# Kernel optimization log

Hardware: AMD Instinct MI355X
Metric: run time of the kernel (lower is better)

Reference implementation:

```python
import jax, jax.numpy as jnp
import numpy as np

N = 8192        # nodes
IN_F = 256      # in_features
OUT_F = 64      # out_features per head
HEADS = 4
ALPHA = 0.2     # leaky relu slope
NEG_INF = -9e15


def setup_inputs() -> dict:
    key = jax.random.key(0)
    ks = jax.random.split(key, 8)
    h = jax.random.normal(ks[0], (N, IN_F), dtype=jnp.float32)
    adj = jax.random.randint(ks[1], (N, N), 0, 2, dtype=jnp.int32)
    # per-head GAT params, stacked over heads
    W = jax.random.normal(ks[2], (HEADS, IN_F, OUT_F), dtype=jnp.float32) * (1.0 / np.sqrt(IN_F))
    a1 = jax.random.normal(ks[3], (HEADS, OUT_F), dtype=jnp.float32) * (1.0 / np.sqrt(OUT_F))
    a2 = jax.random.normal(ks[4], (HEADS, OUT_F), dtype=jnp.float32) * (1.0 / np.sqrt(OUT_F))
    # fusing linear: Linear(out*heads, out)
    fc_w = jax.random.normal(ks[5], (OUT_F, HEADS * OUT_F), dtype=jnp.float32) * (1.0 / np.sqrt(HEADS * OUT_F))
    fc_b = jax.random.normal(ks[6], (OUT_F,), dtype=jnp.float32) * 0.01
    return {"h": h, "adj": adj, "W": W, "a1": a1, "a2": a2, "fc_w": fc_w, "fc_b": fc_b}


def reference(h, adj, W, a1, a2, fc_w, fc_b):
    # all heads batched: Wh [H, N, F]
    Wh = jnp.einsum('ni,hio->hno', h, W)
    # attention logits e_ij = leakyrelu(a1.Wh_i + a2.Wh_j), shape [H, N, N]
    e_src = jnp.einsum('hno,ho->hn', Wh, a1)   # [H, N]
    e_dst = jnp.einsum('hno,ho->hn', Wh, a2)   # [H, N]
    e = jax.nn.leaky_relu(e_src[:, :, None] + e_dst[:, None, :], ALPHA)
    e = jnp.where(adj[None] > 0, e, NEG_INF)
    attn = jax.nn.softmax(e, axis=-1)          # masked softmax over neighbors
    out = jnp.einsum('hnm,hmo->hno', attn, Wh)  # [H, N, F]
    out = jax.nn.elu(out)
    # concat heads along feature dim -> [N, H*F], then fuse linear
    h_concat = jnp.transpose(out, (1, 0, 2)).reshape(N, HEADS * OUT_F)
    return h_concat @ fc_w.T + fc_b
```

## Files before the change

### kernel.cpp

```cpp
#include <hip/hip_runtime.h>
#include <hip/hip_bf16.h>

#define NN 8192
#define NHEADS 4
#define OUTF 64
#define NCHUNK 2
#define CHUNK 4096
#define ROWS 32
#define LOG2E 1.4426950408889634f

typedef __bf16 bf16x8 __attribute__((ext_vector_type(8)));
typedef float fx4 __attribute__((ext_vector_type(4)));
typedef unsigned short ushort8 __attribute__((ext_vector_type(8)));

__global__ __launch_bounds__(256) void k_bits(
    const int* __restrict__ adj, unsigned* __restrict__ bm)
{
  const int lane = threadIdx.x & 63;
  const int row = blockIdx.x * 4 + (threadIdx.x >> 6);
  const int* ap = adj + (size_t)row * NN;
  unsigned* bp = bm + (size_t)row * (NN / 32);

  for (int it8 = 0; it8 < 16; ++it8) {
    int v[8];
#pragma unroll
    for (int u = 0; u < 8; ++u)
      v[u] = ap[(it8 * 8 + u) * 64 + lane];
#pragma unroll
    for (int u = 0; u < 8; ++u) {
      unsigned long long m = __ballot(v[u] != 0);
      unsigned word = (lane == 1) ? (unsigned)(m >> 32) : (unsigned)m;
      if (lane < 2) bp[(it8 * 8 + u) * 2 + lane] = word;
    }
  }
}

__global__ __launch_bounds__(256) void k_wh(
    const float* __restrict__ h, const float* __restrict__ W,
    const float* __restrict__ a1, const float* __restrict__ a2,
    unsigned short* __restrict__ whsw, float* __restrict__ R,
    float* __restrict__ F1, float* __restrict__ F2)
{
  __shared__ float ws[64 * 260];
  const int tid = threadIdx.x;
  const int hd = blockIdx.x >> 7;
  const int i0 = (blockIdx.x & 127) << 6;

  const float* Wp = W + hd * (256 * 64);
  for (int idx = tid; idx < 256 * 64; idx += 256) {
    int k = idx >> 6, o = idx & 63;
    ws[o * 260 + k] = Wp[idx];
  }
  __syncthreads();

  const int w = tid >> 6, o = tid & 63;
  const int ibase = i0 + w * 16;
  float acc[16];
#pragma unroll
  for (int m = 0; m < 16; ++m) acc[m] = 0.f;

  const float* hp = h + (size_t)ibase * 256;
  for (int k4 = 0; k4 < 64; ++k4) {
    fx4 wv = *(const fx4*)(&ws[o * 260 + k4 * 4]);
#pragma unroll
    for (int m = 0; m < 16; ++m) {
      fx4 hv = *(const fx4*)(hp + m * 256 + k4 * 4);
      acc[m] += hv[0] * wv[0] + hv[1] * wv[1] + hv[2] * wv[2] + hv[3] * wv[3];
    }
  }

  const float a1v = a1[hd * 64 + o], a2v = a2[hd * 64 + o];
#pragma unroll
  for (int m = 0; m < 16; ++m) {
    float s1 = acc[m] * a1v, s2 = acc[m] * a2v;
#pragma unroll
    for (int d = 1; d < 64; d <<= 1) {
      s1 += __shfl_xor(s1, d);
      s2 += __shfl_xor(s2, d);
    }
    if (o == 0) {
      int ix = hd * NN + ibase + m;
      R[ix]  = __builtin_amdgcn_exp2f(-0.8f * s1 * LOG2E);
      F1[ix] = __builtin_amdgcn_exp2f(s2 * LOG2E);
      F2[ix] = __builtin_amdgcn_exp2f(0.2f * s2 * LOG2E);
    }
  }

  size_t base = (size_t)hd * 524288 + (size_t)((i0 >> 5) + (w >> 1)) * 2048 +
                (size_t)(o >> 4) * 512;
  int ln0 = (o & 15) + 16 * ((w & 1) * 2);
  ushort8 pk0, pk1;
#pragma unroll
  for (int m = 0; m < 8; ++m) {
    pk0[m] = __builtin_bit_cast(unsigned short, (__bf16)acc[m]);
    pk1[m] = __builtin_bit_cast(unsigned short, (__bf16)acc[m + 8]);
  }
  *(ushort8*)(whsw + base + (size_t)ln0 * 8) = pk0;
  *(ushort8*)(whsw + base + (size_t)(ln0 + 16) * 8) = pk1;
}

struct Tile {
  fx4 f1a, f1b, f2a, f2b;
  bf16x8 b0, b1, b2, b3;
  unsigned m[2];
};

__device__ __forceinline__ void load_tile(Tile& t, const float* F1p,
                                          const float* F2p,
                                          const unsigned short* wp,
                                          const unsigned* bml, int il, int jb)
{
  t.f1a = *(const fx4*)(F1p + jb);
  t.f1b = *(const fx4*)(F1p + jb + 4);
  t.f2a = *(const fx4*)(F2p + jb);
  t.f2b = *(const fx4*)(F2p + jb + 4);
  const unsigned short* wq = wp + (size_t)(jb >> 5) * 2048;
  t.b0 = *(const bf16x8*)(wq);
  t.b1 = *(const bf16x8*)(wq + 512);
  t.b2 = *(const bf16x8*)(wq + 1024);
  t.b3 = *(const bf16x8*)(wq + 1536);
  const int jw = jb >> 5;
  t.m[0] = bml[jw * 32 + (il ^ (jw & 31))];
  t.m[1] = bml[jw * 32 + ((16 + il) ^ (jw & 31))];
}

__device__ __forceinline__ void compute_tile(const Tile& t, const float* Rr,
                                             int g, const bf16x8& ones,
                                             fx4 acc[2][4], fx4* accS)
{
#pragma unroll
  for (int rs = 0; rs < 2; ++rs) {
    unsigned sm = t.m[rs] >> (g * 8);
    float p[8];
#pragma unroll
    for (int e = 0; e < 8; ++e) {
      float f1 = (e < 4) ? t.f1a[e] : t.f1b[e - 4];
      float f2 = (e < 4) ? t.f2a[e] : t.f2b[e - 4];
      float pm = fmaxf(f1, Rr[rs] * f2);
      unsigned keep = (unsigned)(((int)(sm << (31 - e))) >> 31);
      p[e] = __builtin_bit_cast(float,
                 __builtin_bit_cast(unsigned, pm) & keep);
    }
    bf16x8 af;
#pragma unroll
    for (int e = 0; e < 8; ++e) af[e] = (__bf16)p[e];
    acc[rs][0] = __builtin_amdgcn_mfma_f32_16x16x32_bf16(af, t.b0, acc[rs][0], 0, 0, 0);
    acc[rs][1] = __builtin_amdgcn_mfma_f32_16x16x32_bf16(af, t.b1, acc[rs][1], 0, 0, 0);
    acc[rs][2] = __builtin_amdgcn_mfma_f32_16x16x32_bf16(af, t.b2, acc[rs][2], 0, 0, 0);
    acc[rs][3] = __builtin_amdgcn_mfma_f32_16x16x32_bf16(af, t.b3, acc[rs][3], 0, 0, 0);
    accS[rs] = __builtin_amdgcn_mfma_f32_16x16x32_bf16(af, ones, accS[rs], 0, 0, 0);
  }
}

__global__ __launch_bounds__(256) void k_attn(
    const unsigned* __restrict__ bm, const unsigned short* __restrict__ whsw,
    const float* __restrict__ Rg, const float* __restrict__ F1g,
    const float* __restrict__ F2g, float* __restrict__ pacc,
    float* __restrict__ psum)
{
  __shared__ unsigned bml[(CHUNK / 32) * ROWS];
  const int tid = threadIdx.x;
  const int lane = tid & 63;
  const int hd = tid >> 6;
  const int bx = blockIdx.x;
  const int ci = bx & 1;
  const int i0 = (bx >> 1) << 5;
  const int j0 = ci * CHUNK;
  const int il = lane & 15;
  const int g = lane >> 4;

  for (int it = 0; it < 16; ++it) {
    int idx = it * 256 + tid;
    int r = idx >> 7, w = idx & 127;
    unsigned v = bm[(size_t)(i0 + r) * (NN / 32) + (j0 >> 5) + w];
    bml[w * 32 + (r ^ (w & 31))] = v;
  }
  __syncthreads();

  float Rr[2];
#pragma unroll
  for (int rs = 0; rs < 2; ++rs)
    Rr[rs] = Rg[hd * NN + i0 + rs * 16 + il];
  const float* F1p = F1g + hd * NN + j0 + g * 8;
  const float* F2p = F2g + hd * NN + j0 + g * 8;
  const unsigned short* wp = whsw + (size_t)hd * 524288 +
                             (size_t)(j0 >> 5) * 2048 + (size_t)lane * 8;
  bf16x8 ones;
#pragma unroll
  for (int e = 0; e < 8; ++e) ones[e] = (__bf16)1.0f;

  fx4 acc[2][4] = {};
  fx4 accS[2] = {};

  Tile t0, t1;
  load_tile(t0, F1p, F2p, wp, bml, il, 0);
  for (int jb = 0; jb < CHUNK; jb += 64) {
    load_tile(t1, F1p, F2p, wp, bml, il, jb + 32);
    compute_tile(t0, Rr, g, ones, acc, accS);
    if (jb + 64 < CHUNK) load_tile(t0, F1p, F2p, wp, bml, il, jb + 64);
    compute_tile(t1, Rr, g, ones, acc, accS);
  }

#pragma unroll
  for (int rs = 0; rs < 2; ++rs) {
    if (il == 0) {
#pragma unroll
      for (int r = 0; r < 4; ++r)
        psum[(size_t)(ci * NHEADS + hd) * NN + i0 + rs * 16 + g * 4 + r] =
            accS[rs][r];
    }
  }

  float* pc = pacc + (size_t)ci * NN * 256;
#pragma unroll
  for (int rs = 0; rs < 2; ++rs)
#pragma unroll
    for (int r = 0; r < 4; ++r)
#pragma unroll
      for (int ft = 0; ft < 4; ++ft)
        pc[(size_t)(i0 + rs * 16 + g * 4 + r) * 256 + hd * 64 + ft * 16 + il] =
            acc[rs][ft][r];
}

__global__ __launch_bounds__(256) void k_fc(
    const float* __restrict__ pacc, const float* __restrict__ psum,
    const float* __restrict__ fcw, const float* __restrict__ fcb,
    float* __restrict__ out)
{
  __shared__ float ws[256 * 65];
  __shared__ float ash[32 * 260];
  __shared__ float inv[32 * 4];
  const int tid = threadIdx.x;
  const int i0 = blockIdx.x * 32;

  for (int idx = tid; idx < 64 * 256; idx += 256) {
    int o = idx >> 8, c = idx & 255;
    ws[c * 65 + o] = fcw[idx];
  }
  if (tid < 128) {
    int m = tid >> 2, hh = tid & 3;
    float s = 0.f;
#pragma unroll
    for (int ci = 0; ci < NCHUNK; ++ci)
      s += psum[(size_t)(ci * NHEADS + hh) * NN + i0 + m];
    inv[m * 4 + hh] = 1.0f / s;
  }
  __syncthreads();

  for (int idx = tid; idx < 32 * 64; idx += 256) {
    int m = idx >> 6, q = idx & 63;
    int hh = q >> 4;
    size_t off = (size_t)(i0 + m) * 256 + q * 4;
    fx4 v = {};
#pragma unroll
    for (int ci = 0; ci < NCHUNK; ++ci) {
      fx4 a = *(const fx4*)(pacc + (size_t)ci * NN * 256 + off);
      v[0] += a[0]; v[1] += a[1]; v[2] += a[2]; v[3] += a[3];
    }
    float iv = inv[m * 4 + hh];
#pragma unroll
    for (int j = 0; j < 4; ++j) {
      float x = v[j] * iv;
      x = (x > 0.f) ? x : (__builtin_amdgcn_exp2f(x * LOG2E) - 1.0f);
      ash[m * 260 + q * 4 + j] = x;
    }
  }
  __syncthreads();

  const int w = tid >> 6, o = tid & 63;
  float acc[8];
#pragma unroll
  for (int m = 0; m < 8; ++m) acc[m] = 0.f;

  for (int c4 = 0; c4 < 64; ++c4) {
    float w0 = ws[(c4 * 4 + 0) * 65 + o];
    float w1 = ws[(c4 * 4 + 1) * 65 + o];
    float w2 = ws[(c4 * 4 + 2) * 65 + o];
    float w3 = ws[(c4 * 4 + 3) * 65 + o];
#pragma unroll
    for (int m = 0; m < 8; ++m) {
      fx4 hv = *(const fx4*)(&ash[(w * 8 + m) * 260 + c4 * 4]);
      acc[m] += hv[0] * w0 + hv[1] * w1 + hv[2] * w2 + hv[3] * w3;
    }
  }
  const float bo = fcb[o];
#pragma unroll
  for (int m = 0; m < 8; ++m)
    out[(size_t)(i0 + w * 8 + m) * 64 + o] = acc[m] + bo;
}

extern "C" void kernel_launch(void* const* d_in, const int* in_sizes, int n_in,
                              void* d_out, int out_size, void* d_ws, size_t ws_size,
                              hipStream_t stream) {
  (void)in_sizes; (void)n_in; (void)out_size; (void)ws_size;
  const float* h   = (const float*)d_in[0];
  const int*   adj = (const int*)d_in[1];
  const float* W   = (const float*)d_in[2];
  const float* a1  = (const float*)d_in[3];
  const float* a2  = (const float*)d_in[4];
  const float* fcw = (const float*)d_in[5];
  const float* fcb = (const float*)d_in[6];
  float* out = (float*)d_out;

  char* base = (char*)d_ws;
  unsigned short* whsw = (unsigned short*)base;
  float* R  = (float*)(base + (4u << 20));
  float* F1 = (float*)(base + (4u << 20) + (128u << 10));
  float* F2 = (float*)(base + (4u << 20) + (256u << 10));
  unsigned* bmask = (unsigned*)(base + (5u << 20));
  float* pacc = (float*)(base + (13u << 20));
  float* psum = (float*)(base + (29u << 20));

  k_bits<<<dim3(2048), dim3(256), 0, stream>>>(adj, bmask);
  k_wh<<<dim3(512), dim3(256), 0, stream>>>(h, W, a1, a2, whsw, R, F1, F2);
  k_attn<<<dim3(512), dim3(256), 0, stream>>>(bmask, whsw, R, F1, F2, pacc, psum);
  k_fc<<<dim3(256), dim3(256), 0, stream>>>(pacc, psum, fcw, fcb, out);
}
```

Before: 231.6 us.

## Merge prep kernels, split attention into four column chunks with XCD-aware mapping

Fuses the adjacency bit-packing and the Wh projection into one launch, so one kernel launch and its tail are removed. The attention kernel now splits columns into four chunks instead of two, doubling the grid to 1024 blocks for better occupancy. Blocks are remapped so that neighbouring row tiles and chunks land on the same XCD for cache locality. The bitmask LDS layout switches from an XOR swizzle to padding of 33, and W is read from global memory instead of being staged in LDS. The extra chunk doubles the partial-accumulator traffic that k_fc must reduce, and the hidden k_fc code must handle four chunks.

```diff
diff --git a/kernel.cpp b/kernel.cpp
--- a/kernel.cpp
+++ b/kernel.cpp
@@ -4,8 +4,8 @@
 #define NN 8192
 #define NHEADS 4
 #define OUTF 64
-#define NCHUNK 2
-#define CHUNK 4096
+#define NCHUNK 4
+#define CHUNK 2048
 #define ROWS 32
 #define LOG2E 1.4426950408889634f
 
@@ -13,59 +13,56 @@
 typedef float fx4 __attribute__((ext_vector_type(4)));
 typedef unsigned short ushort8 __attribute__((ext_vector_type(8)));
 
-__global__ __launch_bounds__(256) void k_bits(
-    const int* __restrict__ adj, unsigned* __restrict__ bm)
-{
-  const int lane = threadIdx.x & 63;
-  const int row = blockIdx.x * 4 + (threadIdx.x >> 6);
-  const int* ap = adj + (size_t)row * NN;
-  unsigned* bp = bm + (size_t)row * (NN / 32);
-
-  for (int it8 = 0; it8 < 16; ++it8) {
-    int v[8];
-#pragma unroll
-    for (int u = 0; u < 8; ++u)
-      v[u] = ap[(it8 * 8 + u) * 64 + lane];
-#pragma unroll
-    for (int u = 0; u < 8; ++u) {
-      unsigned long long m = __ballot(v[u] != 0);
-      unsigned word = (lane == 1) ? (unsigned)(m >> 32) : (unsigned)m;
-      if (lane < 2) bp[(it8 * 8 + u) * 2 + lane] = word;
-    }
-  }
-}
-
-__global__ __launch_bounds__(256) void k_wh(
+__global__ __launch_bounds__(256) void k_prep(
+    const int* __restrict__ adj, unsigned* __restrict__ bm,
     const float* __restrict__ h, const float* __restrict__ W,
     const float* __restrict__ a1, const float* __restrict__ a2,
     unsigned short* __restrict__ whsw, float* __restrict__ R,
     float* __restrict__ F1, float* __restrict__ F2)
 {
-  __shared__ float ws[64 * 260];
   const int tid = threadIdx.x;
-  const int hd = blockIdx.x >> 7;
-  const int i0 = (blockIdx.x & 127) << 6;
-
-  const float* Wp = W + hd * (256 * 64);
-  for (int idx = tid; idx < 256 * 64; idx += 256) {
-    int k = idx >> 6, o = idx & 63;
-    ws[o * 260 + k] = Wp[idx];
-  }
-  __syncthreads();
-
+  const int bx = blockIdx.x;
+  if (bx < 2048) {
+    const int lane = tid & 63;
+    const int row = bx * 4 + (tid >> 6);
+    const int* ap = adj + (size_t)row * NN;
+    unsigned* bp = bm + (size_t)row * (NN / 32);
+    for (int it8 = 0; it8 < 16; ++it8) {
+      int v[8];
+#pragma unroll
+      for (int u = 0; u < 8; ++u)
+        v[u] = ap[(it8 * 8 + u) * 64 + lane];
+#pragma unroll
+      for (int u = 0; u < 8; ++u) {
+        unsigned long long m = __ballot(v[u] != 0);
+        unsigned word = (lane == 1) ? (unsigned)(m >> 32) : (unsigned)m;
+        if (lane < 2) bp[(it8 * 8 + u) * 2 + lane] = word;
+      }
+    }
+    return;
+  }
+
+  const int b = bx - 2048;
+  const int hd = b >> 7;
+  const int i0 = (b & 127) << 6;
   const int w = tid >> 6, o = tid & 63;
   const int ibase = i0 + w * 16;
+
   float acc[16];
 #pragma unroll
   for (int m = 0; m < 16; ++m) acc[m] = 0.f;
 
   const float* hp = h + (size_t)ibase * 256;
+  const float* Wp = W + hd * (256 * 64) + o;
   for (int k4 = 0; k4 < 64; ++k4) {
-    fx4 wv = *(const fx4*)(&ws[o * 260 + k4 * 4]);
+    float w0 = Wp[(k4 * 4 + 0) * 64];
+    float w1 = Wp[(k4 * 4 + 1) * 64];
+    float w2 = Wp[(k4 * 4 + 2) * 64];
+    float w3 = Wp[(k4 * 4 + 3) * 64];
 #pragma unroll
     for (int m = 0; m < 16; ++m) {
       fx4 hv = *(const fx4*)(hp + m * 256 + k4 * 4);
-      acc[m] += hv[0] * wv[0] + hv[1] * wv[1] + hv[2] * wv[2] + hv[3] * wv[3];
+      acc[m] += hv[0] * w0 + hv[1] * w1 + hv[2] * w2 + hv[3] * w3;
     }
   }
 
@@ -102,7 +99,7 @@
 struct Tile {
   fx4 f1a, f1b, f2a, f2b;
   bf16x8 b0, b1, b2, b3;
-  unsigned m[2];
+  unsigned m0, m1;
 };
 
 __device__ __forceinline__ void load_tile(Tile& t, const float* F1p,
@@ -119,9 +116,9 @@
   t.b1 = *(const bf16x8*)(wq + 512);
   t.b2 = *(const bf16x8*)(wq + 1024);
   t.b3 = *(const bf16x8*)(wq + 1536);
-  const int jw = jb >> 5;
-  t.m[0] = bml[jw * 32 + (il ^ (jw & 31))];
-  t.m[1] = bml[jw * 32 + ((16 + il) ^ (jw & 31))];
+  const unsigned* mb = bml + (jb >> 5) * 33;
+  t.m0 = mb[il];
+  t.m1 = mb[16 + il];
 }
 
 __device__ __forceinline__ void compute_tile(const Tile& t, const float* Rr,
@@ -130,7 +127,7 @@
 {
 #pragma unroll
   for (int rs = 0; rs < 2; ++rs) {
-    unsigned sm = t.m[rs] >> (g * 8);
+    unsigned sm = (rs ? t.m1 : t.m0) >> (g * 8);
     float p[8];
 #pragma unroll
     for (int e = 0; e < 8; ++e) {
@@ -158,22 +155,24 @@
     const float* __restrict__ F2g, float* __restrict__ pacc,
     float* __restrict__ psum)
 {
-  __shared__ unsigned bml[(CHUNK / 32) * ROWS];
+  __shared__ unsigned bml[(CHUNK / 32) * 33];
   const int tid = threadIdx.x;
   const int lane = tid & 63;
   const int hd = tid >> 6;
   const int bx = blockIdx.x;
-  const int ci = bx & 1;
-  const int i0 = (bx >> 1) << 5;
+  const int xcd = bx & 7;
+  const int ci = xcd >> 1;
+  const int rt = ((bx >> 3) << 1) | (xcd & 1);
+  const int i0 = rt << 5;
   const int j0 = ci * CHUNK;
   const int il = lane & 15;
   const int g = lane >> 4;
 
-  for (int it = 0; it < 16; ++it) {
+  for (int it = 0; it < 8; ++it) {
     int idx = it * 256 + tid;
-    int r = idx >> 7, w = idx & 127;
+    int r = idx >> 6, w = idx & 63;
     unsigned v = bm[(size_t)(i0 + r) * (NN / 32) + (j0 >> 5) + w];
-    bml[w * 32 + (r ^ (w & 31))] = v;
+    bml[w * 33 + r] = v;
   }
   __syncthreads();
 
@@ -309,10 +308,10 @@
   float* F2 = (float*)(base + (4u << 20) + (256u << 10));
   unsigned* bmask = (unsigned*)(base + (5u << 20));
   float* pacc = (float*)(base + (13u << 20));
-  float* psum = (float*)(base + (29u << 20));
-
-  k_bits<<<dim3(2048), dim3(256), 0, stream>>>(adj, bmask);
-  k_wh<<<dim3(512), dim3(256), 0, stream>>>(h, W, a1, a2, whsw, R, F1, F2);
-  k_attn<<<dim3(512), dim3(256), 0, stream>>>(bmask, whsw, R, F1, F2, pacc, psum);
+  float* psum = (float*)(base + (45u << 20));
+
+  k_prep<<<dim3(2560), dim3(256), 0, stream>>>(adj, bmask, h, W, a1, a2,
+                                               whsw, R, F1, F2);
+  k_attn<<<dim3(1024), dim3(256), 0, stream>>>(bmask, whsw, R, F1, F2, pacc, psum);
   k_fc<<<dim3(256), dim3(256), 0, stream>>>(pacc, psum, fcw, fcb, out);
 }
```

Result: slower. 290.4 us (+25.4%).
